# Performance work log

Hardware: AMD Instinct MI355X
Metric: run time of the kernel (lower is better)

## Reference

```python
import jax, jax.numpy as jnp
import numpy as np
import math

B, L, D = 4, 4096, 1024
D_EMB, D_HID = 3, 16


def make_pos_emb(emb_dim, seq_len):
    # Complex exponential positional embeddings (non-trainable), shape (1, seq_len, emb_dim)
    t = np.linspace(0.0, 1.0, seq_len, dtype=np.float32)[None, :, None]
    bands = (emb_dim - 1) // 2
    t_res = np.linspace(0.0, seq_len - 1, seq_len, dtype=np.float32)[None, :, None]
    w = 2.0 * math.pi * t_res / seq_len
    f = np.linspace(0.0001, max(bands - 1, 0), bands, dtype=np.float32)[None, None]
    z = np.exp(-1j * (f * w).astype(np.complex64))
    z = np.concatenate([t, z.real.astype(np.float32), z.imag.astype(np.float32)], axis=-1)
    return jnp.asarray(z)


def setup_inputs() -> dict:
    key = jax.random.key(0)
    ks = jax.random.split(key, 8)
    u = jax.random.normal(ks[0], (B, L, D), dtype=jnp.float32)
    z = make_pos_emb(D_EMB, L)  # (1, L, D_EMB)
    # filter MLP: Linear(d_emb, d_hidden) -> ReLU -> Linear(d_hidden, d_model)
    s1 = 1.0 / math.sqrt(D_EMB)
    w1 = jax.random.uniform(ks[1], (D_HID, D_EMB), jnp.float32, -s1, s1)
    b1 = jax.random.uniform(ks[2], (D_HID,), jnp.float32, -s1, s1)
    s2 = 1.0 / math.sqrt(D_HID)
    w2 = jax.random.uniform(ks[3], (D, D_HID), jnp.float32, -s2, s2)
    b2 = jax.random.uniform(ks[4], (D,), jnp.float32, -s2, s2)
    # projection: Linear(d_model, d_model)
    sp = 1.0 / math.sqrt(D)
    pw = jax.random.uniform(ks[5], (D, D), jnp.float32, -sp, sp)
    pb = jax.random.uniform(ks[6], (D,), jnp.float32, -sp, sp)
    return {"u": u, "z": z, "w1": w1, "b1": b1, "w2": w2, "b2": b2, "pw": pw, "pb": pb}


def fft_conv(u_bdl, k_dl):
    # u_bdl: (B, D, L), k_dl: (1, D, L) or (D, L)
    seqlen = u_bdl.shape[-1]
    fft_size = 2 * seqlen
    k_f = jnp.fft.rfft(k_dl, n=fft_size) / fft_size
    u_f = jnp.fft.rfft(u_bdl, n=fft_size)
    y = jnp.fft.irfft(u_f * k_f, n=fft_size, norm="forward")[..., :seqlen]
    return y


def reference(u, z, w1, b1, w2, b2, pw, pb):
    seqlen = u.shape[1]
    pe = z[:, :seqlen]  # (1, L, D_EMB)
    h = jax.nn.relu(jnp.einsum("ble,he->blh", pe, w1) + b1)
    filt = jnp.einsum("blh,dh->bld", h, w2) + b2  # (1, L, D)
    filt = jnp.transpose(filt, (0, 2, 1))  # (1, D, L)
    u_conv = fft_conv(jnp.transpose(u, (0, 2, 1)), filt)  # (B, D, L)
    u_conv = jnp.transpose(u_conv, (0, 2, 1)).astype(u.dtype)  # (B, L, D)
    u_proj = jnp.einsum("bld,od->blo", u, pw) + pb
    return u_conv * u_proj + u
```

## Files before the change

### kernel.cpp

```cpp
#include <hip/hip_runtime.h>
#include <hip/hip_bf16.h>

#define SEQL 4096
#define DCH  1024
#define BATCH 4
#define KH   4097

typedef __attribute__((ext_vector_type(2))) float cf;
__device__ __forceinline__ cf mkc(float x, float y){ cf r; r.x = x; r.y = y; return r; }
__device__ __forceinline__ cf cadd(cf a, cf b){ return a + b; }
__device__ __forceinline__ cf csub(cf a, cf b){ return a - b; }
__device__ __forceinline__ cf cmul(cf a, cf b){ return a.xx * b + mkc(-a.y, a.y) * b.yx; }
__device__ __forceinline__ cf cconjf(cf a){ return mkc(a.x, -a.y); }
__device__ __forceinline__ cf addi(cf a, cf b){ return a + mkc(-b.y, b.x); }
__device__ __forceinline__ cf subi(cf a, cf b){ return a - mkc(-b.y, b.x); }
__device__ __forceinline__ int phi(int c){ return c ^ ((c >> 4) & 15); }
__device__ __forceinline__ int drev(int i){
    return ((i>>10)&3) | (((i>>8)&3)<<2) | (((i>>6)&3)<<4)
         | (((i>>4)&3)<<6) | (((i>>2)&3)<<8) | ((i&3)<<10);
}

__device__ __forceinline__ cf W1c(int j){
    const float cs[4] = {1.f, 0.92387953f, 0.70710678f, 0.38268343f};
    const float sn[4] = {0.f, -0.38268343f, -0.70710678f, -0.92387953f};
    return mkc(cs[j], sn[j]);
}
__device__ __forceinline__ cf W2c(int j){
    const float cs[4] = {1.f, 0.70710678f, 0.f, -0.70710678f};
    const float sn[4] = {0.f, -0.70710678f, -1.f, -0.70710678f};
    return mkc(cs[j], sn[j]);
}
__device__ __forceinline__ cf W3c(int j){
    const float cs[4] = {1.f, 0.38268343f, -0.70710678f, -0.92387953f};
    const float sn[4] = {0.f, -0.92387953f, -0.70710678f, 0.38268343f};
    return mkc(cs[j], sn[j]);
}

__device__ __forceinline__ unsigned pack2bf(float a, float b){
    unsigned r;
    asm("v_cvt_pk_bf16_f32 %0, %1, %2" : "=v"(r) : "v"(a), "v"(b));
    return r;
}
__device__ __forceinline__ float bflo(unsigned u){ return __uint_as_float(u << 16); }
__device__ __forceinline__ float bfhi(unsigned u){ return __uint_as_float(u & 0xffff0000u); }

__device__ __forceinline__ void gload16(const void* g, void* l){
    __builtin_amdgcn_global_load_lds((const __attribute__((address_space(1))) void*)g,
                                     (__attribute__((address_space(3))) void*)l, 16, 0, 0);
}

__global__ __launch_bounds__(256) void twiddle_init(cf* __restrict__ tw4, cf* __restrict__ tw8){
    int i = blockIdx.x*256 + threadIdx.x;
    const double TWO_PI = 6.283185307179586476925286766559;
    double a4 = -TWO_PI * (double)i / 4096.0;
    double a8 = -TWO_PI * (double)i / 8192.0;
    tw4[i] = mkc((float)cos(a4), (float)sin(a4));
    tw8[i] = mkc((float)cos(a8), (float)sin(a8));
}

__global__ __launch_bounds__(256) void mlp_kernel(
        const float* __restrict__ z, const float* __restrict__ w1,
        const float* __restrict__ b1, float* __restrict__ h) {
    int l = blockIdx.x * blockDim.x + threadIdx.x;
    if (l >= SEQL) return;
    float pe0 = z[l * 3 + 0], pe1 = z[l * 3 + 1], pe2 = z[l * 3 + 2];
#pragma unroll
    for (int j = 0; j < 16; ++j) {
        float v = pe0 * w1[j * 3 + 0] + pe1 * w1[j * 3 + 1] + pe2 * w1[j * 3 + 2] + b1[j];
        h[l * 16 + j] = v > 0.f ? v : 0.f;
    }
}

__global__ __launch_bounds__(256) void transpose_kernel(
        const float* __restrict__ u, unsigned* __restrict__ utb,
        unsigned short* __restrict__ ub) {
    __shared__ float tile[32][33];
    int b = blockIdx.z;
    int l0 = blockIdx.x * 32;
    int d0 = blockIdx.y * 32;
    int tx = threadIdx.x, ty = threadIdx.y;
    const float* up = u + (size_t)b * SEQL * DCH;
    unsigned short* ubp = ub ? ub + (size_t)b * SEQL * DCH : (unsigned short*)0;
#pragma unroll
    for (int i = 0; i < 32; i += 8) {
        size_t idx = (size_t)(l0 + ty + i) * DCH + d0 + tx;
        float v = up[idx];
        tile[ty + i][tx] = v;
        if (ub) ubp[idx] = (unsigned short)pack2bf(v, v);
    }
    __syncthreads();
    unsigned* utp = utb + (size_t)b * DCH * (SEQL / 2);
    int t  = ty * 32 + tx;
    int dl = t >> 4;
    int lp = t & 15;
#pragma unroll
    for (int p = 0; p < 2; ++p) {
        int dd = dl + p * 16;
        unsigned v = pack2bf(tile[2 * lp][dd], tile[2 * lp + 1][dd]);
        utp[(size_t)(d0 + dd) * (SEQL / 2) + (l0 >> 1) + lp] = v;
    }
}

__global__ __launch_bounds__(256) void pw2bf_kernel(
        const float* __restrict__ pw, unsigned short* __restrict__ pwb) {
    int t = blockIdx.x * 256 + threadIdx.x;
    float4 a = *(const float4*)&pw[(size_t)t * 8];
    float4 b = *(const float4*)&pw[(size_t)t * 8 + 4];
    uint4 o;
    o.x = pack2bf(a.x, a.y); o.y = pack2bf(a.z, a.w);
    o.z = pack2bf(b.x, b.y); o.w = pack2bf(b.z, b.w);
    *(uint4*)&pwb[(size_t)t * 8] = o;
}

__device__ void dif_mid_and_chunk(cf* lds, const cf* __restrict__ tw){
    const int tid = threadIdx.x;
#pragma unroll
    for (int p = 1; p < 4; ++p) {
        const int lm = 10 - 2*p;
        const int m  = 1 << lm;
        const int step = 1024 >> lm;
#pragma unroll
        for (int it = 0; it < 4; ++it) {
            int j = tid + (it << 8);
            int k = j & (m-1);
            int g = j >> lm;
            int i0 = (g << (lm+2)) + k;
            cf x0 = lds[phi(i0)];
            cf x1 = lds[phi(i0+m)];
            cf x2 = lds[phi(i0+2*m)];
            cf x3 = lds[phi(i0+3*m)];
            cf b0 = cadd(x0,x2), b1 = csub(x0,x2);
            cf b2 = cadd(x1,x3), b3 = csub(x1,x3);
            cf u0 = cadd(b0,b2);
            cf u2 = csub(b0,b2);
            cf u1 = subi(b1,b3);
            cf u3 = addi(b1,b3);
            int t1 = k*step;
            lds[phi(i0)]     = u0;
            lds[phi(i0+m)]   = cmul(u1, tw[t1]);
            lds[phi(i0+2*m)] = cmul(u2, tw[2*t1]);
            lds[phi(i0+3*m)] = cmul(u3, tw[3*t1]);
        }
        __syncthreads();
    }
    {
        const int b0 = tid << 4;
        const int xr = tid & 15;
        cf v[16];
#pragma unroll
        for (int j=0;j<16;++j) v[j] = lds[b0 + (j ^ xr)];
#pragma unroll
        for (int j=0;j<4;++j){
            cf x0=v[j], x1=v[j+4], x2=v[j+8], x3=v[j+12];
            cf b0v=cadd(x0,x2), b1=csub(x0,x2), b2=cadd(x1,x3), b3=csub(x1,x3);
            cf u0=cadd(b0v,b2), u2=csub(b0v,b2), u1=subi(b1,b3), u3=addi(b1,b3);
            v[j]    = u0;
            v[j+4]  = cmul(u1, W1c(j));
            v[j+8]  = cmul(u2, W2c(j));
            v[j+12] = cmul(u3, W3c(j));
        }
#pragma unroll
        for (int c=0;c<4;++c){
            cf x0=v[4*c], x1=v[4*c+1], x2=v[4*c+2], x3=v[4*c+3];
            cf b0v=cadd(x0,x2), b1=csub(x0,x2), b2=cadd(x1,x3), b3=csub(x1,x3);
            v[4*c]   = cadd(b0v,b2);
            v[4*c+1] = subi(b1,b3);
            v[4*c+2] = csub(b0v,b2);
            v[4*c+3] = addi(b1,b3);
        }
#pragma unroll
        for (int j=0;j<16;++j) lds[b0 + (j ^ xr)] = v[j];
        __syncthreads();
    }
}

__device__ void dit_chunk_and_mid(cf* lds, const cf* __restrict__ tw){
    const int tid = threadIdx.x;
    {
        const int b0 = tid << 4;
        const int xr = tid & 15;
        cf v[16];
#pragma unroll
        for (int j=0;j<16;++j) v[j] = lds[b0 + (j ^ xr)];
#pragma unroll
        for (int c=0;c<4;++c){
            cf a0=v[4*c], a1=v[4*c+1], a2=v[4*c+2], a3=v[4*c+3];
            cf b0v=cadd(a0,a2), b1=csub(a0,a2), b2=cadd(a1,a3), b3=csub(a1,a3);
            v[4*c]   = cadd(b0v,b2);
            v[4*c+1] = addi(b1,b3);
            v[4*c+2] = csub(b0v,b2);
            v[4*c+3] = subi(b1,b3);
        }
#pragma unroll
        for (int j=0;j<4;++j){
            cf a0=v[j];
            cf a1=cmul(v[j+4],  cconjf(W1c(j)));
            cf a2=cmul(v[j+8],  cconjf(W2c(j)));
            cf a3=cmul(v[j+12], cconjf(W3c(j)));
            cf b0v=cadd(a0,a2), b1=csub(a0,a2), b2=cadd(a1,a3), b3=csub(a1,a3);
            v[j]    = cadd(b0v,b2);
            v[j+4]  = addi(b1,b3);
            v[j+8]  = csub(b0v,b2);
            v[j+12] = subi(b1,b3);
        }
#pragma unroll
        for (int j=0;j<16;++j) lds[b0 + (j ^ xr)] = v[j];
        __syncthreads();
    }
#pragma unroll
    for (int p = 0; p < 3; ++p) {
        const int lm = 4 + 2*p;
        const int m  = 1 << lm;
        const int step = 1024 >> lm;
#pragma unroll
        for (int it = 0; it < 4; ++it) {
            int j = tid + (it << 8);
            int k = j & (m-1);
            int g = j >> lm;
            int i0 = (g << (lm+2)) + k;
            int t1 = k*step;
            cf a0 = lds[phi(i0)];
            cf a1 = cmul(lds[phi(i0+m)],   cconjf(tw[t1]));
            cf a2 = cmul(lds[phi(i0+2*m)], cconjf(tw[2*t1]));
            cf a3 = cmul(lds[phi(i0+3*m)], cconjf(tw[3*t1]));
            cf b0=cadd(a0,a2), b1=csub(a0,a2), b2=cadd(a1,a3), b3=csub(a1,a3);
            lds[phi(i0)]     = cadd(b0,b2);
            lds[phi(i0+m)]   = addi(b1,b3);
            lds[phi(i0+2*m)] = csub(b0,b2);
            lds[phi(i0+3*m)] = subi(b1,b3);
        }
        __syncthreads();
    }
}

__global__ __launch_bounds__(256) void filt_fft_kernel(
        const float* __restrict__ h, const float* __restrict__ w2,
        const float* __restrict__ b2, const cf* __restrict__ tw4,
        const cf* __restrict__ tw8, cf* __restrict__ kf) {
    __shared__ cf lds[4096];
    const int d = blockIdx.x;
    const int tid = threadIdx.x;
    float wv[16];
#pragma unroll
    for (int j = 0; j < 16; ++j) wv[j] = w2[d * 16 + j];
    const float bb = b2[d];
#pragma unroll
    for (int it = 0; it < 4; ++it) {
        int j = tid + (it << 8);
        const float* h0 = h + (size_t)(2*j) * 16;
        const float* h1 = h + (size_t)(2*(j+1024)) * 16;
        float f0 = bb, f1 = bb, f2 = bb, f3 = bb;
#pragma unroll
        for (int i = 0; i < 16; ++i) {
            f0 += h0[i] * wv[i];  f1 += h0[16+i] * wv[i];
            f2 += h1[i] * wv[i];  f3 += h1[16+i] * wv[i];
        }
        cf x0 = mkc(f0, f1), x1 = mkc(f2, f3);
        cf u0 = cadd(x0,x1);
        cf u2 = csub(x0,x1);
        cf u1 = subi(x0,x1);
        cf u3 = addi(x0,x1);
        lds[phi(j)]      = u0;
        lds[phi(j+1024)] = cmul(u1, tw4[j]);
        lds[phi(j+2048)] = cmul(u2, tw4[2*j]);
        lds[phi(j+3072)] = cmul(u3, tw4[3*j]);
    }
    __syncthreads();
    dif_mid_and_chunk(lds, tw4);
    const float s = 1.f / 8192.f;
    cf* Hrow = kf + (size_t)d * KH;
    const int lane  = tid & 63;
    const int kbase = ((lane & 31) << 6) | ((lane >> 5) << 5) | ((tid >> 6) << 3);
#pragma unroll
    for (int it = 0; it < 8; ++it) {
        int k = kbase + it;
        if (k == 0) {
            cf c0 = lds[0];
            Hrow[0]    = mkc((c0.x + c0.y) * s, 0.f);
            Hrow[4096] = mkc((c0.x - c0.y) * s, 0.f);
            cf c2 = lds[phi(drev(2048))];
            Hrow[2048] = mkc(c2.x * s, -c2.y * s);
        } else {
            int kk = 4096 - k;
            cf ck  = lds[phi(drev(k))];
            cf ckk = lds[phi(drev(kk))];
            cf cc = cconjf(ckk);
            cf E  = (ck + cc) * 0.5f;
            cf Dd = csub(ck, cc);
            cf O  = mkc(Dd.y, -Dd.x) * 0.5f;
            cf wvv = tw8[k];
            cf Xk  = cadd(E, cmul(wvv, O));
            cf wp  = mkc(-wvv.x, wvv.y);
            cf Xkk = cadd(cconjf(E), cmul(wp, cconjf(O)));
            Hrow[k]  = Xk * s;
            Hrow[kk] = Xkk * s;
        }
    }
}

__global__ __launch_bounds__(256) void conv_kernel(
        unsigned* __restrict__ utyb, const cf* __restrict__ tw4,
        const cf* __restrict__ tw8, const cf* __restrict__ kf) {
    __shared__ cf lds[4096];
    const int row = blockIdx.x;
    const int d = row & (DCH - 1);
    const int tid = threadIdx.x;
    unsigned* rp = utyb + (size_t)row * (SEQL / 2);
#pragma unroll
    for (int it = 0; it < 4; ++it) {
        int j = tid + (it << 8);
        unsigned q0 = rp[j], q1 = rp[j + 1024];
        cf x0 = mkc(bflo(q0), bfhi(q0));
        cf x1 = mkc(bflo(q1), bfhi(q1));
        cf u0 = cadd(x0,x1);
        cf u2 = csub(x0,x1);
        cf u1 = subi(x0,x1);
        cf u3 = addi(x0,x1);
        lds[phi(j)]      = u0;
        lds[phi(j+1024)] = cmul(u1, tw4[j]);
        lds[phi(j+2048)] = cmul(u2, tw4[2*j]);
        lds[phi(j+3072)] = cmul(u3, tw4[3*j]);
    }
    __syncthreads();
    dif_mid_and_chunk(lds, tw4);
    const cf* Hrow = kf + (size_t)d * KH;
    {
        const int lane  = tid & 63;
        const int kbase = ((lane & 31) << 6) | ((lane >> 5) << 5) | ((tid >> 6) << 3);
#pragma unroll
        for (int it = 0; it < 8; ++it) {
            int k = kbase + it;
            if (k == 0) {
                cf c0 = lds[0];
                float X0 = c0.x + c0.y, X4 = c0.x - c0.y;
                cf H0 = Hrow[0], H4 = Hrow[4096];
                cf Y0 = H0 * X0;
                cf Y4 = H4 * X4;
                cf S  = cadd(Y0, Y4), Dd = csub(Y0, Y4);
                lds[0] = addi(S, Dd);
                int s2 = phi(drev(2048));
                cf c2 = lds[s2];
                cf Y2 = cmul(cconjf(c2), Hrow[2048]);
                lds[s2] = mkc(2.f * Y2.x, -2.f * Y2.y);
            } else {
                int kk = 4096 - k;
                int sk = phi(drev(k)), skk = phi(drev(kk));
                cf ck = lds[sk], ckk = lds[skk];
                cf cc = cconjf(ckk);
                cf E  = (ck + cc) * 0.5f;
                cf Dd = csub(ck, cc);
                cf O  = mkc(Dd.y, -Dd.x) * 0.5f;
                cf wv = tw8[k];
                cf Xk  = cadd(E, cmul(wv, O));
                cf wp  = mkc(-wv.x, wv.y);
                cf Xkk = cadd(cconjf(E), cmul(wp, cconjf(O)));
                cf Yk  = cmul(Xk,  Hrow[k]);
                cf Ykk = cmul(Xkk, Hrow[kk]);
                cf cy = cconjf(Ykk);
                cf S  = cadd(Yk, cy), D2 = csub(Yk, cy);
                cf Zk = addi(S, cmul(cconjf(wv), D2));
                cf cy2 = cconjf(Yk);
                cf S2  = cadd(Ykk, cy2), D3 = csub(Ykk, cy2);
                cf Zkk = subi(S2, cmul(wv, D3));
                lds[sk] = Zk; lds[skk] = Zkk;
            }
        }
    }
    __syncthreads();
    dit_chunk_and_mid(lds, tw4);
#pragma unroll
    for (int it = 0; it < 4; ++it) {
        int j = tid + (it << 8);
        cf a0 = lds[phi(j)];
        cf a1 = cmul(lds[phi(j+1024)], cconjf(tw4[j]));
        cf a2 = cmul(lds[phi(j+2048)], cconjf(tw4[2*j]));
        cf a3 = cmul(lds[phi(j+3072)], cconjf(tw4[3*j]));
        cf b0 = cadd(a0,a2), b1 = csub(a0,a2);
        cf b2 = cadd(a1,a3), b3 = csub(a1,a3);
        cf o0 = cadd(b0,b2);
        cf o1 = addi(b1,b3);
        rp[j]        = pack2bf(o0.x, o0.y);
        rp[j + 1024] = pack2bf(o1.x, o1.y);
    }
}

typedef __attribute__((ext_vector_type(8))) short short8;
typedef __attribute__((ext_vector_type(4))) float f32x4;

__global__ __launch_bounds__(256, 4) void gemm_mfma_v2(
        const unsigned short* __restrict__ ub, const unsigned short* __restrict__ pwb,
        const float* __restrict__ pb, const unsigned short* __restrict__ yb,
        float* __restrict__ out) {
    __shared__ char lds_raw[34816];
    float (*ysc)[132] = (float(*)[132])lds_raw;

    const int tid  = threadIdx.x;
    const int lane = tid & 63;
    const int wid  = tid >> 6;
    const int wr   = wid >> 1;
    const int wc   = wid & 1;
    const int m0   = blockIdx.x * 128;
    const int n0   = blockIdx.y * 128;

    f32x4 acc[4][4] = {};

    const int srow = lane >> 2;
    const int scol = 16 * ((lane & 3) ^ ((lane >> 2) & 3));

#define STAGE2(bufbase, kt)                                                                   \
    {                                                                                         \
        _Pragma("unroll")                                                                     \
        for (int i = 0; i < 2; ++i) {                                                         \
            int c = wid * 2 + i;                                                              \
            const char* gA = (const char*)ub  + (size_t)(m0 + c * 16 + srow) * 2048 + (kt) * 2 + scol; \
            const char* gB = (const char*)pwb + (size_t)(n0 + c * 16 + srow) * 2048 + (kt) * 2 + scol; \
            gload16(gA, lds_raw + (bufbase) + c * 1024);                                      \
            gload16(gB, lds_raw + (bufbase) + 8192 + c * 1024);                               \
        }                                                                                     \
    }

    STAGE2(0, 0);
    __syncthreads();

    for (int t = 0; t < 32; ++t) {
        const int cur = (t & 1) << 14;
        if (t < 31) STAGE2(cur ^ 16384, (t + 1) * 32);
        short8 af[4], bfr[4];
#pragma unroll
        for (int f = 0; f < 4; ++f) {
            int rowA = wr * 64 + f * 16 + (lane & 15);
            int rowB = wc * 64 + f * 16 + (lane & 15);
            int offA = cur + rowA * 64 + (((lane >> 4) * 16) ^ ((rowA & 3) << 4));
            int offB = cur + 8192 + rowB * 64 + (((lane >> 4) * 16) ^ ((rowB & 3) << 4));
            af[f]  = *(short8*)(lds_raw + offA);
            bfr[f] = *(short8*)(lds_raw + offB);
        }
#pragma unroll
        for (int mf = 0; mf < 4; ++mf)
#pragma unroll
            for (int nf = 0; nf < 4; ++nf)
                acc[mf][nf] = __builtin_amdgcn_mfma_f32_16x16x32_bf16(
                    af[mf], bfr[nf], acc[mf][nf], 0, 0, 0);
        __syncthreads();
    }

    const int b  = m0 >> 12;
    const int l0 = m0 & (SEQL - 1);
    float pbv[4];
#pragma unroll
    for (int nf = 0; nf < 4; ++nf)
        pbv[nf] = pb[n0 + wc * 64 + nf * 16 + (lane & 15)];

    for (int c = 0; c < 2; ++c) {
        __syncthreads();
#pragma unroll
        for (int j = 0; j < 4; ++j) {
            int idx = j * 256 + tid;
            int dn  = idx >> 3;
            int lg  = idx & 7;
            uint4 w4 = *(const uint4*)&yb[(((size_t)(b * DCH + n0 + dn)) << 12) + l0 + c * 64 + lg * 8];
            int lb = lg * 8;
            ysc[lb+0][dn] = bflo(w4.x); ysc[lb+1][dn] = bfhi(w4.x);
            ysc[lb+2][dn] = bflo(w4.y); ysc[lb+3][dn] = bfhi(w4.y);
            ysc[lb+4][dn] = bflo(w4.z); ysc[lb+5][dn] = bfhi(w4.z);
            ysc[lb+6][dn] = bflo(w4.w); ysc[lb+7][dn] = bfhi(w4.w);
        }
        __syncthreads();
        if (wr == c) {
#pragma unroll
            for (int mf = 0; mf < 4; ++mf)
#pragma unroll
                for (int i = 0; i < 4; ++i) {
                    int lrow = mf * 16 + (lane >> 4) * 4 + i;
                    int m = m0 + c * 64 + lrow;
#pragma unroll
                    for (int nf = 0; nf < 4; ++nf) {
                        int nl = wc * 64 + nf * 16 + (lane & 15);
                        int n = n0 + nl;
                        float proj = acc[mf][nf][i] + pbv[nf];
                        float ures = __uint_as_float((unsigned)ub[(size_t)m * DCH + n] << 16);
                        out[(size_t)m * DCH + n] = ysc[lrow][nl] * proj + ures;
                    }
                }
        }
    }
#undef STAGE2
}

__global__ __launch_bounds__(256, 3) void gemm_mfma_fb(
        const float* __restrict__ u, const float* __restrict__ pw,
        const float* __restrict__ pb, const unsigned short* __restrict__ yb,
        float* __restrict__ out) {
    __shared__ char lds_raw[34816];
    float (*ysc)[132] = (float(*)[132])lds_raw;
    const int tid  = threadIdx.x;
    const int lane = tid & 63;
    const int wid  = tid >> 6;
    const int wr   = wid >> 1;
    const int wc   = wid & 1;
    const int m0   = blockIdx.x * 128;
    const int n0   = blockIdx.y * 128;
    f32x4 acc[4][4] = {};
    float4 ra[4], rb[4];
    int s_row[4], s_f4[4];
#pragma unroll
    for (int j = 0; j < 4; ++j) {
        int idx = j * 256 + tid;
        s_row[j] = idx >> 3;
        s_f4[j]  = idx & 7;
    }
#define LOADT(kt)                                                                     \
    {                                                                                 \
        _Pragma("unroll")                                                             \
        for (int j = 0; j < 4; ++j) {                                                 \
            ra[j] = *(const float4*)&u [(size_t)(m0 + s_row[j]) * DCH + (kt) + s_f4[j] * 4]; \
            rb[j] = *(const float4*)&pw[(size_t)(n0 + s_row[j]) * DCH + (kt) + s_f4[j] * 4]; \
        }                                                                             \
    }
#define WRITET(base)                                                                  \
    {                                                                                 \
        _Pragma("unroll")                                                             \
        for (int j = 0; j < 4; ++j) {                                                 \
            int off = (base) + ((s_row[j] * 64 + s_f4[j] * 8) ^ ((s_row[j] & 3) << 4)); \
            uint2 pa, pbv2;                                                           \
            pa.x   = pack2bf(ra[j].x, ra[j].y);  pa.y   = pack2bf(ra[j].z, ra[j].w);  \
            pbv2.x = pack2bf(rb[j].x, rb[j].y);  pbv2.y = pack2bf(rb[j].z, rb[j].w);  \
            *(uint2*)(lds_raw + off)        = pa;                                     \
            *(uint2*)(lds_raw + off + 8192) = pbv2;                                   \
        }                                                                             \
    }
    LOADT(0);
    WRITET(0);
    LOADT(32);
    __syncthreads();
    for (int t = 0; t < 32; ++t) {
        const int cur = (t & 1) << 14;
        short8 af[4], bfr[4];
#pragma unroll
        for (int f = 0; f < 4; ++f) {
            int rowA = wr * 64 + f * 16 + (lane & 15);
            int rowB = wc * 64 + f * 16 + (lane & 15);
            int offA = cur + ((rowA * 64 + ((lane >> 4) * 16)) ^ ((rowA & 3) << 4));
            int offB = cur + 8192 + ((rowB * 64 + ((lane >> 4) * 16)) ^ ((rowB & 3) << 4));
            af[f]  = *(short8*)(lds_raw + offA);
            bfr[f] = *(short8*)(lds_raw + offB);
        }
        if (t < 31) WRITET(cur ^ 16384);
        if (t < 30) LOADT((t + 2) * 32);
#pragma unroll
        for (int mf = 0; mf < 4; ++mf)
#pragma unroll
            for (int nf = 0; nf < 4; ++nf)
                acc[mf][nf] = __builtin_amdgcn_mfma_f32_16x16x32_bf16(
                    af[mf], bfr[nf], acc[mf][nf], 0, 0, 0);
        __syncthreads();
    }
    const int b  = m0 >> 12;
    const int l0 = m0 & (SEQL - 1);
    float pbv[4];
#pragma unroll
    for (int nf = 0; nf < 4; ++nf)
        pbv[nf] = pb[n0 + wc * 64 + nf * 16 + (lane & 15)];
    for (int c = 0; c < 2; ++c) {
        __syncthreads();
#pragma unroll
        for (int j = 0; j < 4; ++j) {
            int idx = j * 256 + tid;
            int dn  = idx >> 3;
            int lg  = idx & 7;
            uint4 w4 = *(const uint4*)&yb[(((size_t)(b * DCH + n0 + dn)) << 12) + l0 + c * 64 + lg * 8];
            int lb = lg * 8;
            ysc[lb+0][dn] = bflo(w4.x); ysc[lb+1][dn] = bfhi(w4.x);
            ysc[lb+2][dn] = bflo(w4.y); ysc[lb+3][dn] = bfhi(w4.y);
            ysc[lb+4][dn] = bflo(w4.z); ysc[lb+5][dn] = bfhi(w4.z);
            ysc[lb+6][dn] = bflo(w4.w); ysc[lb+7][dn] = bfhi(w4.w);
        }
        __syncthreads();
        if (wr == c) {
#pragma unroll
            for (int mf = 0; mf < 4; ++mf)
#pragma unroll
                for (int i = 0; i < 4; ++i) {
                    int lrow = mf * 16 + (lane >> 4) * 4 + i;
                    int m = m0 + c * 64 + lrow;
#pragma unroll
                    for (int nf = 0; nf < 4; ++nf) {
                        int nl = wc * 64 + nf * 16 + (lane & 15);
                        int n = n0 + nl;
                        float proj = acc[mf][nf][i] + pbv[nf];
                        out[(size_t)m * DCH + n] = ysc[lrow][nl] * proj + u[(size_t)m * DCH + n];
                    }
                }
        }
    }
#undef LOADT
#undef WRITET
}

extern "C" void kernel_launch(void* const* d_in, const int* in_sizes, int n_in,
                              void* d_out, int out_size, void* d_ws, size_t ws_size,
                              hipStream_t stream) {
    const float* u  = (const float*)d_in[0];
    const float* z  = (const float*)d_in[1];
    const float* w1 = (const float*)d_in[2];
    const float* b1 = (const float*)d_in[3];
    const float* w2 = (const float*)d_in[4];
    const float* b2 = (const float*)d_in[5];
    const float* pw = (const float*)d_in[6];
    const float* pb = (const float*)d_in[7];
    float* out = (float*)d_out;

    float*    h    = (float*)d_ws;
    unsigned* utyb = (unsigned*)((char*)d_ws + 262144);
    cf* kf = (cf*)d_out;

    const size_t ub_off  = 262144 + (size_t)BATCH * DCH * (SEQL / 2) * sizeof(unsigned);
    const size_t pwb_off = ub_off + (size_t)BATCH * SEQL * DCH * sizeof(unsigned short);
    const size_t tw_off  = pwb_off + (size_t)DCH * DCH * sizeof(unsigned short);
    const size_t need    = tw_off + 2 * 4096 * sizeof(cf);
    const bool   big     = ws_size >= need;

    cf* tw4 = big ? (cf*)((char*)d_ws + tw_off) : (cf*)((char*)d_out + (40u << 20));
    cf* tw8 = tw4 + 4096;
    unsigned short* ub  = big ? (unsigned short*)((char*)d_ws + ub_off)  : (unsigned short*)0;
    unsigned short* pwb = big ? (unsigned short*)((char*)d_ws + pwb_off) : (unsigned short*)0;

    twiddle_init<<<dim3(16), dim3(256), 0, stream>>>(tw4, tw8);
    mlp_kernel<<<dim3(16), dim3(256), 0, stream>>>(z, w1, b1, h);
    transpose_kernel<<<dim3(SEQL / 32, DCH / 32, BATCH), dim3(32, 8), 0, stream>>>(u, utyb, ub);
    if (big) pw2bf_kernel<<<dim3(512), dim3(256), 0, stream>>>(pw, pwb);
    filt_fft_kernel<<<dim3(DCH), dim3(256), 0, stream>>>(h, w2, b2, tw4, tw8, kf);
    conv_kernel<<<dim3(BATCH * DCH), dim3(256), 0, stream>>>(utyb, tw4, tw8, kf);
    if (big)
        gemm_mfma_v2<<<dim3(128, 8), dim3(256), 0, stream>>>(ub, pwb, pb, (const unsigned short*)utyb, out);
    else
        gemm_mfma_fb<<<dim3(128, 8), dim3(256), 0, stream>>>(u, pw, pb, (const unsigned short*)utyb, out);
}
```

Measured before the change: 266.4 us.

## Rewrite projection GEMM with 256x128 tiles and triple-buffered 64-wide K stages

Replaces the 128x128, 256-thread, double-buffered projection GEMM with a 512-thread kernel. It computes a 256x128 output tile per block and keeps three 64-wide K stages in a ~144KB LDS ring. Global loads for stage t+2 are interleaved with the MFMA sub-quadrants of stage t, using explicit vmcnt/lgkmcnt waits, s_barrier and setprio to overlap memory with compute. The aim is to cut per-K-step barrier overhead and improve operand reuse. The large LDS footprint limits the GPU to one block per CU, and the epilogue is reworked to stage 128 rows of the conv output at a time.

```diff
diff --git a/kernel.cpp b/kernel.cpp
--- a/kernel.cpp
+++ b/kernel.cpp
@@ -387,11 +387,11 @@
 typedef __attribute__((ext_vector_type(8))) short short8;
 typedef __attribute__((ext_vector_type(4))) float f32x4;
 
-__global__ __launch_bounds__(256, 4) void gemm_mfma_v2(
+__global__ __launch_bounds__(512, 2) void gemm_mfma_v3(
         const unsigned short* __restrict__ ub, const unsigned short* __restrict__ pwb,
         const float* __restrict__ pb, const unsigned short* __restrict__ yb,
         float* __restrict__ out) {
-    __shared__ char lds_raw[34816];
+    __shared__ char lds_raw[147456];
     float (*ysc)[132] = (float(*)[132])lds_raw;
 
     const int tid  = threadIdx.x;
@@ -399,51 +399,84 @@
     const int wid  = tid >> 6;
     const int wr   = wid >> 1;
     const int wc   = wid & 1;
-    const int m0   = blockIdx.x * 128;
+    const int m0   = blockIdx.x * 256;
     const int n0   = blockIdx.y * 128;
 
     f32x4 acc[4][4] = {};
 
-    const int srow = lane >> 2;
-    const int scol = 16 * ((lane & 3) ^ ((lane >> 2) & 3));
-
-#define STAGE2(bufbase, kt)                                                                   \
-    {                                                                                         \
-        _Pragma("unroll")                                                                     \
-        for (int i = 0; i < 2; ++i) {                                                         \
-            int c = wid * 2 + i;                                                              \
-            const char* gA = (const char*)ub  + (size_t)(m0 + c * 16 + srow) * 2048 + (kt) * 2 + scol; \
-            const char* gB = (const char*)pwb + (size_t)(n0 + c * 16 + srow) * 2048 + (kt) * 2 + scol; \
-            gload16(gA, lds_raw + (bufbase) + c * 1024);                                      \
-            gload16(gB, lds_raw + (bufbase) + 8192 + c * 1024);                               \
-        }                                                                                     \
-    }
-
-    STAGE2(0, 0);
+#pragma unroll
+    for (int tt = 0; tt < 2; ++tt) {
+#pragma unroll
+        for (int un = 0; un < 3; ++un) {
+            const unsigned short* gs = (un == 2) ? pwb : ub;
+            int growb = (un == 2) ? n0 : (m0 + un * 128);
+#pragma unroll
+            for (int j = 0; j < 2; ++j) {
+                int rr = j * 64 + (tid >> 3);
+                int ss = (tid & 7) ^ ((tid >> 3) & 7);
+                gload16(gs + (size_t)(growb + rr) * 1024 + tt * 64 + ss * 8,
+                        lds_raw + tt * 49152 + un * 16384 + rr * 128 + (tid & 7) * 16);
+            }
+        }
+    }
+    asm volatile("s_waitcnt vmcnt(6)" ::: "memory");
+    __builtin_amdgcn_sched_barrier(0);
+    __builtin_amdgcn_s_barrier();
+
+    for (int t = 0; t < 16; ++t) {
+        const int Ab  = (t % 3) * 49152;
+        const int Bb  = Ab + 32768;
+        const int sbB = ((t + 2) % 3) * 49152;
+        const int kt2 = (t + 2) * 64;
+#pragma unroll
+        for (int q = 0; q < 4; ++q) {
+            const int qr = q >> 1, qc = q & 1;
+            short8 af[2][2], bfr[2][2];
+#pragma unroll
+            for (int f = 0; f < 2; ++f) {
+                int arow = wr * 64 + qr * 32 + f * 16 + (lane & 15);
+                int brow = wc * 64 + qc * 32 + f * 16 + (lane & 15);
+#pragma unroll
+                for (int kh = 0; kh < 2; ++kh) {
+                    int ks = (lane >> 4) + 4 * kh;
+                    af[f][kh]  = *(short8*)(lds_raw + Ab + arow * 128 + (ks ^ (arow & 7)) * 16);
+                    bfr[f][kh] = *(short8*)(lds_raw + Bb + brow * 128 + (ks ^ (brow & 7)) * 16);
+                }
+            }
+            if (q < 3 && t < 14) {
+                const unsigned short* gs = (q == 2) ? pwb : ub;
+                int growb = (q == 2) ? n0 : (m0 + q * 128);
+#pragma unroll
+                for (int j = 0; j < 2; ++j) {
+                    int rr = j * 64 + (tid >> 3);
+                    int ss = (tid & 7) ^ ((tid >> 3) & 7);
+                    gload16(gs + (size_t)(growb + rr) * 1024 + kt2 + ss * 8,
+                            lds_raw + sbB + q * 16384 + rr * 128 + (tid & 7) * 16);
+                }
+            }
+            __builtin_amdgcn_s_barrier();
+            asm volatile("s_waitcnt lgkmcnt(0)" ::: "memory");
+            __builtin_amdgcn_sched_barrier(0);
+            __builtin_amdgcn_s_setprio(1);
+#pragma unroll
+            for (int fa = 0; fa < 2; ++fa)
+#pragma unroll
+                for (int fb = 0; fb < 2; ++fb)
+#pragma unroll
+                    for (int kh = 0; kh < 2; ++kh)
+                        acc[qr * 2 + fa][qc * 2 + fb] = __builtin_amdgcn_mfma_f32_16x16x32_bf16(
+                            af[fa][kh], bfr[fb][kh], acc[qr * 2 + fa][qc * 2 + fb], 0, 0, 0);
+            __builtin_amdgcn_s_setprio(0);
+            if (q == 3) {
+                if (t < 14)       asm volatile("s_waitcnt vmcnt(6)" ::: "memory");
+                else if (t == 14) asm volatile("s_waitcnt vmcnt(0)" ::: "memory");
+                __builtin_amdgcn_sched_barrier(0);
+            }
+            __builtin_amdgcn_s_barrier();
+        }
+    }
+
     __syncthreads();
-
-    for (int t = 0; t < 32; ++t) {
-        const int cur = (t & 1) << 14;
-        if (t < 31) STAGE2(cur ^ 16384, (t + 1) * 32);
-        short8 af[4], bfr[4];
-#pragma unroll
-        for (int f = 0; f < 4; ++f) {
-            int rowA = wr * 64 + f * 16 + (lane & 15);
-            int rowB = wc * 64 + f * 16 + (lane & 15);
-            int offA = cur + rowA * 64 + (((lane >> 4) * 16) ^ ((rowA & 3) << 4));
-            int offB = cur + 8192 + rowB * 64 + (((lane >> 4) * 16) ^ ((rowB & 3) << 4));
-            af[f]  = *(short8*)(lds_raw + offA);
-            bfr[f] = *(short8*)(lds_raw + offB);
-        }
-#pragma unroll
-        for (int mf = 0; mf < 4; ++mf)
-#pragma unroll
-            for (int nf = 0; nf < 4; ++nf)
-                acc[mf][nf] = __builtin_amdgcn_mfma_f32_16x16x32_bf16(
-                    af[mf], bfr[nf], acc[mf][nf], 0, 0, 0);
-        __syncthreads();
-    }
-
     const int b  = m0 >> 12;
     const int l0 = m0 & (SEQL - 1);
     float pbv[4];
@@ -453,26 +486,28 @@
 
     for (int c = 0; c < 2; ++c) {
         __syncthreads();
-#pragma unroll
-        for (int j = 0; j < 4; ++j) {
-            int idx = j * 256 + tid;
-            int dn  = idx >> 3;
-            int lg  = idx & 7;
-            uint4 w4 = *(const uint4*)&yb[(((size_t)(b * DCH + n0 + dn)) << 12) + l0 + c * 64 + lg * 8];
-            int lb = lg * 8;
-            ysc[lb+0][dn] = bflo(w4.x); ysc[lb+1][dn] = bfhi(w4.x);
-            ysc[lb+2][dn] = bflo(w4.y); ysc[lb+3][dn] = bfhi(w4.y);
-            ysc[lb+4][dn] = bflo(w4.z); ysc[lb+5][dn] = bfhi(w4.z);
-            ysc[lb+6][dn] = bflo(w4.w); ysc[lb+7][dn] = bfhi(w4.w);
-        }
-        __syncthreads();
-        if (wr == c) {
+        {
+            int dn = tid >> 2;
+            int lq = tid & 3;
+            const uint4* uptr = (const uint4*)(yb + (((size_t)(b * DCH + n0 + dn)) << 12) + l0 + c * 128);
+#pragma unroll
+            for (int jj = 0; jj < 4; ++jj) {
+                uint4 w4 = uptr[lq * 4 + jj];
+                int lb = (lq * 4 + jj) * 8;
+                ysc[lb+0][dn] = bflo(w4.x); ysc[lb+1][dn] = bfhi(w4.x);
+                ysc[lb+2][dn] = bflo(w4.y); ysc[lb+3][dn] = bfhi(w4.y);
+                ysc[lb+4][dn] = bflo(w4.z); ysc[lb+5][dn] = bfhi(w4.z);
+                ysc[lb+6][dn] = bflo(w4.w); ysc[lb+7][dn] = bfhi(w4.w);
+            }
+        }
+        __syncthreads();
+        if ((wr >> 1) == c) {
 #pragma unroll
             for (int mf = 0; mf < 4; ++mf)
 #pragma unroll
                 for (int i = 0; i < 4; ++i) {
-                    int lrow = mf * 16 + (lane >> 4) * 4 + i;
-                    int m = m0 + c * 64 + lrow;
+                    int lrow = (wr & 1) * 64 + mf * 16 + (lane >> 4) * 4 + i;
+                    int m = m0 + c * 128 + lrow;
 #pragma unroll
                     for (int nf = 0; nf < 4; ++nf) {
                         int nl = wc * 64 + nf * 16 + (lane & 15);
@@ -484,7 +519,6 @@
                 }
         }
     }
-#undef STAGE2
 }
 
 __global__ __launch_bounds__(256, 3) void gemm_mfma_fb(
@@ -632,7 +666,7 @@
     filt_fft_kernel<<<dim3(DCH), dim3(256), 0, stream>>>(h, w2, b2, tw4, tw8, kf);
     conv_kernel<<<dim3(BATCH * DCH), dim3(256), 0, stream>>>(utyb, tw4, tw8, kf);
     if (big)
-        gemm_mfma_v2<<<dim3(128, 8), dim3(256), 0, stream>>>(ub, pwb, pb, (const unsigned short*)utyb, out);
+        gemm_mfma_v3<<<dim3(64, 8), dim3(512), 0, stream>>>(ub, pwb, pb, (const unsigned short*)utyb, out);
     else
         gemm_mfma_fb<<<dim3(128, 8), dim3(256), 0, stream>>>(u, pw, pb, (const unsigned short*)utyb, out);
 }
```

Result: no change. 263.2 us (-1.2%).
